# Kernel optimization log

Hardware: AMD Instinct MI355X
Metric: run time of the kernel (lower is better)

## Reference

```python
import jax, jax.numpy as jnp
import numpy as np

N_NODES = 50000
N_EDGES = 800000
N_GRAPHS = 512
F_IN = 9
H = 64
H2 = 32


def gcn_conv(x, W, b, edge_index, num_nodes):
    # PyG GCNConv: add self loops, sym-normalize, x @ W, scatter-add, + bias
    src, dst = edge_index[0], edge_index[1]
    xw = x @ W  # [N, out]
    deg = 1.0 + jax.ops.segment_sum(jnp.ones_like(src, dtype=xw.dtype), dst,
                                    num_segments=num_nodes)  # self-loop adds 1
    dis = jax.lax.rsqrt(deg)  # deg >= 1
    norm = dis[src] * dis[dst]  # [E]
    out = jax.ops.segment_sum(xw[src] * norm[:, None], dst, num_segments=num_nodes)
    out = out + xw * (dis * dis)[:, None]  # self-loop contribution
    return out + b


def edge_conv(x, W, b, edge_index, num_nodes):
    # PyG EdgeConv with nn = Linear(2*in, out) + ReLU, aggr='max'
    src, dst = edge_index[0], edge_index[1]
    xi = x[dst]
    xj = x[src]
    h = jax.nn.relu(jnp.concatenate([xi, xj - xi], axis=-1) @ W + b)  # [E, out]
    agg = jax.ops.segment_max(h, dst, num_segments=num_nodes)
    return jnp.where(jnp.isfinite(agg), agg, 0.0)  # empty segments -> 0


def setup_inputs() -> dict:
    key = jax.random.key(0)
    ks = jax.random.split(key, 16)
    x = jax.random.normal(ks[0], (N_NODES, F_IN), dtype=jnp.float32)
    edge_index = jax.random.randint(ks[1], (2, N_EDGES), 0, N_NODES, dtype=jnp.int32)
    adj = jax.random.randint(ks[2], (2, N_EDGES), 0, N_NODES, dtype=jnp.int32)
    batch = jnp.sort(jax.random.randint(ks[3], (N_NODES,), 0, N_GRAPHS, dtype=jnp.int32))
    s = lambda fan_in: 1.0 / np.sqrt(fan_in)
    W1 = jax.random.uniform(ks[4], (F_IN, H), jnp.float32, -s(F_IN), s(F_IN))
    b1 = jnp.zeros((H,), jnp.float32)
    eW1 = jax.random.uniform(ks[5], (2 * H, H), jnp.float32, -s(2 * H), s(2 * H))
    eb1 = jnp.zeros((H,), jnp.float32)
    W2 = jax.random.uniform(ks[6], (H, H2), jnp.float32, -s(H), s(H))
    b2 = jnp.zeros((H2,), jnp.float32)
    eW2 = jax.random.uniform(ks[7], (2 * H2, H2), jnp.float32, -s(2 * H2), s(2 * H2))
    eb2 = jnp.zeros((H2,), jnp.float32)
    fcW = jax.random.uniform(ks[8], (H2, 1), jnp.float32, -s(H2), s(H2))
    fcb = jax.random.uniform(ks[9], (1,), jnp.float32, -s(H2), s(H2))
    return {"x": x, "edge_index": edge_index, "adj": adj, "batch": batch,
            "W1": W1, "b1": b1, "eW1": eW1, "eb1": eb1,
            "W2": W2, "b2": b2, "eW2": eW2, "eb2": eb2,
            "fcW": fcW, "fcb": fcb}


def reference(x, edge_index, adj, batch, W1, b1, eW1, eb1, W2, b2, eW2, eb2, fcW, fcb):
    n = x.shape[0]
    h = jax.nn.relu(gcn_conv(x, W1, b1, edge_index, n))
    h = jax.nn.relu(edge_conv(h, eW1, eb1, adj, n))
    h = jax.nn.relu(gcn_conv(h, W2, b2, edge_index, n))
    h = jax.nn.relu(edge_conv(h, eW2, eb2, adj, n))
    h = h @ fcW + fcb  # [N, 1]
    # global_mean_pool
    sums = jax.ops.segment_sum(h, batch, num_segments=N_GRAPHS)
    cnts = jax.ops.segment_sum(jnp.ones((n, 1), h.dtype), batch, num_segments=N_GRAPHS)
    return sums / jnp.maximum(cnts, 1.0)
```

## Files before the change

### kernel.cpp

```cpp
#include <hip/hip_runtime.h>
#include <math.h>

#define NN 50000
#define NE 800000
#define NG 512
#define FIN 9
#define D1 64
#define D2 32
#define PAD 64

static inline int cdiv(int a, int b) { return (a + b - 1) / b; }

__global__ void k_scatter(const int* __restrict__ ei, const int* __restrict__ adj,
                          int* __restrict__ deg_e, int* __restrict__ slot_e,
                          int* __restrict__ deg_a, int* __restrict__ slot_a) {
  int e = blockIdx.x * blockDim.x + threadIdx.x;
  if (e >= NE) return;
  int s = ei[e], d = ei[NE + e];
  int p = atomicAdd(&deg_e[d], 1);
  if (p < PAD) slot_e[(size_t)d * PAD + p] = s;
  s = adj[e];
  d = adj[NE + e];
  p = atomicAdd(&deg_a[d], 1);
  if (p < PAD) slot_a[(size_t)d * PAD + p] = s;
}

__global__ void k_xw1(const float* __restrict__ x, const float* __restrict__ W1,
                      const int* __restrict__ deg_e, float* __restrict__ dis,
                      float* __restrict__ xws1) {
  int gid = blockIdx.x * blockDim.x + threadIdx.x;
  int i = gid >> 6, j = gid & 63;
  if (i >= NN) return;
  float di = rsqrtf(1.0f + (float)deg_e[i]);
  if (j == 0) dis[i] = di;
  const float* xr = x + i * FIN;
  float acc = 0.f;
#pragma unroll
  for (int k = 0; k < FIN; ++k) acc += xr[k] * W1[k * D1 + j];
  xws1[i * D1 + j] = acc * di;
}

template <int FI, int FOT, int MODE, bool SCALE>
__global__ __launch_bounds__(256) void k_gemm(const float* __restrict__ H,
                                              const float* __restrict__ W,
                                              const float* __restrict__ dis,
                                              float* __restrict__ OA,
                                              float* __restrict__ OB) {
  constexpr int TM = 4;
  constexpr int TN = (FOT >= 64) ? 4 : 2;
  constexpr int BN = 1024 * TN / FOT;
  constexpr int LDH = BN + 1;
  constexpr int FO = FOT / 2;
  __shared__ float ht[FI][LDH];
  __shared__ float wc[FI][FOT];

  for (int t = threadIdx.x; t < FI * FOT; t += 256) {
    int k = t / FOT, j = t % FOT;
    float v;
    if (MODE == 1)
      v = (j < FO) ? W[k * FO + j] : W[(FI + k) * FO + (j - FO)];
    else
      v = W[k * FOT + j];
    wc[k][j] = v;
  }
  int node0 = blockIdx.x * BN;
  for (int t = threadIdx.x; t < BN * FI; t += 256) {
    int n = t / FI, k = t % FI;
    int nn = node0 + n;
    ht[k][n] = (nn < NN) ? H[(size_t)nn * FI + k] : 0.f;
  }
  __syncthreads();

  int tn = threadIdx.x % (FOT / TN);
  int tm = threadIdx.x / (FOT / TN);
  int j0 = tn * TN, n0 = tm * TM;

  float acc[TM][TN];
#pragma unroll
  for (int m = 0; m < TM; ++m)
#pragma unroll
    for (int q = 0; q < TN; ++q) acc[m][q] = 0.f;

  for (int k = 0; k < FI; ++k) {
    float wv[TN];
    if (TN == 4) {
      float4 w4 = *(const float4*)&wc[k][j0];
      wv[0] = w4.x; wv[1] = w4.y; wv[2] = w4.z; wv[3] = w4.w;
    } else {
      float2 w2 = *(const float2*)&wc[k][j0];
      wv[0] = w2.x; wv[1] = w2.y;
    }
    float hv[TM];
#pragma unroll
    for (int m = 0; m < TM; ++m) hv[m] = ht[k][n0 + m];
#pragma unroll
    for (int m = 0; m < TM; ++m)
#pragma unroll
      for (int q = 0; q < TN; ++q) acc[m][q] += hv[m] * wv[q];
  }

#pragma unroll
  for (int m = 0; m < TM; ++m) {
    int n = node0 + n0 + m;
    if (n >= NN) break;
    float sc = SCALE ? dis[n] : 1.0f;
    float* dst;
    if (MODE == 1)
      dst = (j0 < FO) ? (OA + (size_t)n * FO + j0) : (OB + (size_t)n * FO + (j0 - FO));
    else
      dst = OA + (size_t)n * FOT + j0;
    if (TN == 4) {
      float4 o = {acc[m][0] * sc, acc[m][1] * sc, acc[m][2] * sc, acc[m][3] * sc};
      *(float4*)dst = o;
    } else {
      float2 o = {acc[m][0] * sc, acc[m][1] * sc};
      *(float2*)dst = o;
    }
  }
}

template <int F>
__global__ void k_gcn4(const float4* __restrict__ xws, const float* __restrict__ dis,
                       const int* __restrict__ deg, const int* __restrict__ slots,
                       const float* __restrict__ b, float4* __restrict__ hout) {
  constexpr int L = F / 4;
  int gid = blockIdx.x * blockDim.x + threadIdx.x;
  int i = gid / L, l = gid % L;
  if (i >= NN) return;
  const int* s = slots + (size_t)i * PAD;
  int n = deg[i];
  float4 acc = xws[(size_t)i * L + l];
  int t = 0;
  for (; t + 7 < n; t += 8) {
    int i0 = s[t], i1 = s[t + 1], i2 = s[t + 2], i3 = s[t + 3];
    int i4 = s[t + 4], i5 = s[t + 5], i6 = s[t + 6], i7 = s[t + 7];
    float4 v0 = xws[(size_t)i0 * L + l];
    float4 v1 = xws[(size_t)i1 * L + l];
    float4 v2 = xws[(size_t)i2 * L + l];
    float4 v3 = xws[(size_t)i3 * L + l];
    float4 v4 = xws[(size_t)i4 * L + l];
    float4 v5 = xws[(size_t)i5 * L + l];
    float4 v6 = xws[(size_t)i6 * L + l];
    float4 v7 = xws[(size_t)i7 * L + l];
    acc.x += ((v0.x + v1.x) + (v2.x + v3.x)) + ((v4.x + v5.x) + (v6.x + v7.x));
    acc.y += ((v0.y + v1.y) + (v2.y + v3.y)) + ((v4.y + v5.y) + (v6.y + v7.y));
    acc.z += ((v0.z + v1.z) + (v2.z + v3.z)) + ((v4.z + v5.z) + (v6.z + v7.z));
    acc.w += ((v0.w + v1.w) + (v2.w + v3.w)) + ((v4.w + v5.w) + (v6.w + v7.w));
  }
  for (; t < n; ++t) {
    float4 v = xws[(size_t)s[t] * L + l];
    acc.x += v.x; acc.y += v.y; acc.z += v.z; acc.w += v.w;
  }
  float di = dis[i];
  float4 bb = ((const float4*)b)[l];
  float4 o;
  o.x = fmaxf(bb.x + di * acc.x, 0.f);
  o.y = fmaxf(bb.y + di * acc.y, 0.f);
  o.z = fmaxf(bb.z + di * acc.z, 0.f);
  o.w = fmaxf(bb.w + di * acc.w, 0.f);
  hout[(size_t)i * L + l] = o;
}

template <int F>
__global__ void k_edge4(const float4* __restrict__ A, const float4* __restrict__ B,
                        const float* __restrict__ eb, const int* __restrict__ deg,
                        const int* __restrict__ slots, float4* __restrict__ hout) {
  constexpr int L = F / 4;
  int gid = blockIdx.x * blockDim.x + threadIdx.x;
  int i = gid / L, l = gid % L;
  if (i >= NN) return;
  const int* s = slots + (size_t)i * PAD;
  int n = deg[i];
  float4 M = {-INFINITY, -INFINITY, -INFINITY, -INFINITY};
  int t = 0;
  for (; t + 7 < n; t += 8) {
    int i0 = s[t], i1 = s[t + 1], i2 = s[t + 2], i3 = s[t + 3];
    int i4 = s[t + 4], i5 = s[t + 5], i6 = s[t + 6], i7 = s[t + 7];
    float4 v0 = B[(size_t)i0 * L + l];
    float4 v1 = B[(size_t)i1 * L + l];
    float4 v2 = B[(size_t)i2 * L + l];
    float4 v3 = B[(size_t)i3 * L + l];
    float4 v4 = B[(size_t)i4 * L + l];
    float4 v5 = B[(size_t)i5 * L + l];
    float4 v6 = B[(size_t)i6 * L + l];
    float4 v7 = B[(size_t)i7 * L + l];
    M.x = fmaxf(M.x, fmaxf(fmaxf(fmaxf(v0.x, v1.x), fmaxf(v2.x, v3.x)),
                           fmaxf(fmaxf(v4.x, v5.x), fmaxf(v6.x, v7.x))));
    M.y = fmaxf(M.y, fmaxf(fmaxf(fmaxf(v0.y, v1.y), fmaxf(v2.y, v3.y)),
                           fmaxf(fmaxf(v4.y, v5.y), fmaxf(v6.y, v7.y))));
    M.z = fmaxf(M.z, fmaxf(fmaxf(fmaxf(v0.z, v1.z), fmaxf(v2.z, v3.z)),
                           fmaxf(fmaxf(v4.z, v5.z), fmaxf(v6.z, v7.z))));
    M.w = fmaxf(M.w, fmaxf(fmaxf(fmaxf(v0.w, v1.w), fmaxf(v2.w, v3.w)),
                           fmaxf(fmaxf(v4.w, v5.w), fmaxf(v6.w, v7.w))));
  }
  for (; t < n; ++t) {
    float4 v = B[(size_t)s[t] * L + l];
    M.x = fmaxf(M.x, v.x); M.y = fmaxf(M.y, v.y);
    M.z = fmaxf(M.z, v.z); M.w = fmaxf(M.w, v.w);
  }
  float4 a = A[(size_t)i * L + l];
  float4 bsl = B[(size_t)i * L + l];
  float4 e4 = ((const float4*)eb)[l];
  float4 o;
  o.x = fmaxf(a.x - bsl.x + e4.x + M.x, 0.f);
  o.y = fmaxf(a.y - bsl.y + e4.y + M.y, 0.f);
  o.z = fmaxf(a.z - bsl.z + e4.z + M.z, 0.f);
  o.w = fmaxf(a.w - bsl.w + e4.w + M.w, 0.f);
  hout[(size_t)i * L + l] = o;
}

__global__ void k_final(const float* __restrict__ h4, const float* __restrict__ fcW,
                        const float* __restrict__ fcb, const int* __restrict__ batch,
                        float* __restrict__ sums, float* __restrict__ cnt) {
  int i = blockIdx.x * blockDim.x + threadIdx.x;
  int lane = threadIdx.x & 63;
  bool valid = (i < NN);
  float val = 0.f, c = 0.f;
  int g = -1;
  if (valid) {
    float acc = fcb[0];
#pragma unroll
    for (int k = 0; k < D2; ++k) acc += h4[(size_t)i * D2 + k] * fcW[k];
    val = acc;
    c = 1.f;
    g = batch[i];
  }
#pragma unroll
  for (int d = 1; d < 64; d <<= 1) {
    float v2 = __shfl_down(val, d);
    float c2 = __shfl_down(c, d);
    int g2 = __shfl_down(g, d);
    if (lane + d < 64 && g2 == g) {
      val += v2;
      c += c2;
    }
  }
  int gprev = __shfl_up(g, 1);
  bool is_head = (lane == 0) || (gprev != g);
  if (valid && is_head) {
    atomicAdd(&sums[g], val);
    atomicAdd(&cnt[g], c);
  }
}

__global__ void k_out(const float* __restrict__ sums, const float* __restrict__ cnt,
                      float* __restrict__ out) {
  int g = blockIdx.x * blockDim.x + threadIdx.x;
  if (g < NG) out[g] = sums[g] / fmaxf(cnt[g], 1.0f);
}

extern "C" void kernel_launch(void* const* d_in, const int* in_sizes, int n_in,
                              void* d_out, int out_size, void* d_ws, size_t ws_size,
                              hipStream_t stream) {
  const float* x = (const float*)d_in[0];
  const int* ei = (const int*)d_in[1];
  const int* adj = (const int*)d_in[2];
  const int* batch = (const int*)d_in[3];
  const float* W1 = (const float*)d_in[4];
  const float* b1 = (const float*)d_in[5];
  const float* eW1 = (const float*)d_in[6];
  const float* eb1 = (const float*)d_in[7];
  const float* W2 = (const float*)d_in[8];
  const float* b2 = (const float*)d_in[9];
  const float* eW2 = (const float*)d_in[10];
  const float* eb2 = (const float*)d_in[11];
  const float* fcW = (const float*)d_in[12];
  const float* fcb = (const float*)d_in[13];
  float* out = (float*)d_out;

  char* ws = (char*)d_ws;
  size_t p = 0;
  auto alloc = [&](size_t bytes) -> void* {
    void* r = ws + p;
    p = (p + bytes + 255) & ~(size_t)255;
    return r;
  };
  int* deg_e = (int*)alloc(NN * 4);
  int* deg_a = (int*)alloc(NN * 4);
  float* sums = (float*)alloc(NG * 4);
  float* cnt = (float*)alloc(NG * 4);
  size_t zero_bytes = p;
  int* slot_e = (int*)alloc((size_t)NN * PAD * 4);
  int* slot_a = (int*)alloc((size_t)NN * PAD * 4);
  float* dis = (float*)alloc(NN * 4);
  float* buf0 = (float*)alloc((size_t)NN * D1 * 4);
  float* buf1 = (float*)alloc((size_t)NN * D1 * 4);
  float* buf2 = (float*)alloc((size_t)NN * D1 * 4);
  float* buf3 = (float*)alloc((size_t)NN * D1 * 4);

  hipMemsetAsync(d_ws, 0, zero_bytes, stream);

  k_scatter<<<cdiv(NE, 256), 256, 0, stream>>>(ei, adj, deg_e, slot_e, deg_a, slot_a);

  k_xw1<<<cdiv(NN * D1, 256), 256, 0, stream>>>(x, W1, deg_e, dis, buf0);
  k_gcn4<D1><<<cdiv(NN * (D1 / 4), 256), 256, 0, stream>>>(
      (const float4*)buf0, dis, deg_e, slot_e, b1, (float4*)buf1);

  k_gemm<D1, 2 * D1, 1, false><<<cdiv(NN, 32), 256, 0, stream>>>(buf1, eW1, nullptr, buf2, buf3);
  k_edge4<D1><<<cdiv(NN * (D1 / 4), 256), 256, 0, stream>>>(
      (const float4*)buf2, (const float4*)buf3, eb1, deg_a, slot_a, (float4*)buf0);

  k_gemm<D1, D2, 0, true><<<cdiv(NN, 64), 256, 0, stream>>>(buf0, W2, dis, buf1, nullptr);
  k_gcn4<D2><<<cdiv(NN * (D2 / 4), 256), 256, 0, stream>>>(
      (const float4*)buf1, dis, deg_e, slot_e, b2, (float4*)buf3);

  float* A2 = buf2;
  float* B2 = buf2 + (size_t)NN * D2;
  k_gemm<D2, 2 * D2, 1, false><<<cdiv(NN, 64), 256, 0, stream>>>(buf3, eW2, nullptr, A2, B2);
  k_edge4<D2><<<cdiv(NN * (D2 / 4), 256), 256, 0, stream>>>(
      (const float4*)A2, (const float4*)B2, eb2, deg_a, slot_a, (float4*)buf1);

  k_final<<<cdiv(NN, 256), 256, 0, stream>>>(buf1, fcW, fcb, batch, sums, cnt);
  k_out<<<cdiv(NG, 256), 256, 0, stream>>>(sums, cnt, out);
}
```

Before: 390.0 us.

## Build adjacency via atomic linked lists then convert to padded slot arrays

Replaces the atomicAdd scatter, which wrote each source index into a random slot, with two steps. First, atomicExch builds a per-destination linked list of edge ids. Second, one thread per node walks its list and writes the slots contiguously. This aims to turn scattered slot writes into per-node sequential writes. In exchange it adds an extra kernel, a pointer-chasing walk with serialized dependent loads, extra next arrays and a second memset. Neighbour order within a node also changes, which could alter float summation order slightly.

New measurement: 388.4 us. Within noise of the previous version (-0.4%).

```diff
diff --git a/kernel.cpp b/kernel.cpp
--- a/kernel.cpp
+++ b/kernel.cpp
@@ -8,21 +8,41 @@
 #define D1 64
 #define D2 32
 #define PAD 64
+#define NN2 (2 * NN)
 
 static inline int cdiv(int a, int b) { return (a + b - 1) / b; }
 
-__global__ void k_scatter(const int* __restrict__ ei, const int* __restrict__ adj,
+__global__ void k_build(const int* __restrict__ ei, const int* __restrict__ adj,
+                        int* __restrict__ head_e, int* __restrict__ next_e,
+                        int* __restrict__ head_a, int* __restrict__ next_a) {
+  int e = blockIdx.x * blockDim.x + threadIdx.x;
+  if (e < NE) {
+    int d1 = ei[NE + e];
+    next_e[e] = atomicExch(&head_e[d1], e);
+    int d2 = adj[NE + e];
+    next_a[e] = atomicExch(&head_a[d2], e);
+  }
+}
+
+__global__ void k_convert(const int* __restrict__ head_e, const int* __restrict__ next_e,
+                          const int* __restrict__ head_a, const int* __restrict__ next_a,
+                          const int* __restrict__ ei, const int* __restrict__ adj,
                           int* __restrict__ deg_e, int* __restrict__ slot_e,
                           int* __restrict__ deg_a, int* __restrict__ slot_a) {
-  int e = blockIdx.x * blockDim.x + threadIdx.x;
-  if (e >= NE) return;
-  int s = ei[e], d = ei[NE + e];
-  int p = atomicAdd(&deg_e[d], 1);
-  if (p < PAD) slot_e[(size_t)d * PAD + p] = s;
-  s = adj[e];
-  d = adj[NE + e];
-  p = atomicAdd(&deg_a[d], 1);
-  if (p < PAD) slot_a[(size_t)d * PAD + p] = s;
+  int t = blockIdx.x * blockDim.x + threadIdx.x;
+  if (t >= NN2) return;
+  bool isE = t < NN;
+  int i = isE ? t : t - NN;
+  int e = isE ? head_e[i] : head_a[i];
+  const int* nxt = isE ? next_e : next_a;
+  const int* sv = isE ? ei : adj;
+  int* slot = (isE ? slot_e : slot_a) + (size_t)i * PAD;
+  int p = 0;
+  while (e >= 0 && p < PAD) {
+    slot[p++] = sv[e];
+    e = nxt[e];
+  }
+  (isE ? deg_e : deg_a)[i] = p;
 }
 
 __global__ void k_xw1(const float* __restrict__ x, const float* __restrict__ W1,
@@ -275,11 +295,16 @@
     p = (p + bytes + 255) & ~(size_t)255;
     return r;
   };
+  int* head_e = (int*)alloc(NN * 4);
+  int* head_a = (int*)alloc(NN * 4);
+  size_t ff_bytes = p;
+  float* sums = (float*)alloc(NG * 4);
+  float* cnt = (float*)alloc(NG * 4);
+  size_t zero_end = p;
+  int* next_e = (int*)alloc(NE * 4);
+  int* next_a = (int*)alloc(NE * 4);
   int* deg_e = (int*)alloc(NN * 4);
   int* deg_a = (int*)alloc(NN * 4);
-  float* sums = (float*)alloc(NG * 4);
-  float* cnt = (float*)alloc(NG * 4);
-  size_t zero_bytes = p;
   int* slot_e = (int*)alloc((size_t)NN * PAD * 4);
   int* slot_a = (int*)alloc((size_t)NN * PAD * 4);
   float* dis = (float*)alloc(NN * 4);
@@ -288,9 +313,12 @@
   float* buf2 = (float*)alloc((size_t)NN * D1 * 4);
   float* buf3 = (float*)alloc((size_t)NN * D1 * 4);
 
-  hipMemsetAsync(d_ws, 0, zero_bytes, stream);
-
-  k_scatter<<<cdiv(NE, 256), 256, 0, stream>>>(ei, adj, deg_e, slot_e, deg_a, slot_a);
+  hipMemsetAsync(d_ws, 0xFF, ff_bytes, stream);
+  hipMemsetAsync(ws + ff_bytes, 0, zero_end - ff_bytes, stream);
+
+  k_build<<<cdiv(NE, 256), 256, 0, stream>>>(ei, adj, head_e, next_e, head_a, next_a);
+  k_convert<<<cdiv(NN2, 256), 256, 0, stream>>>(head_e, next_e, head_a, next_a, ei, adj,
+                                                deg_e, slot_e, deg_a, slot_a);
 
   k_xw1<<<cdiv(NN * D1, 256), 256, 0, stream>>>(x, W1, deg_e, dis, buf0);
   k_gcn4<D1><<<cdiv(NN * (D1 / 4), 256), 256, 0, stream>>>(
```
